# Kernel tuning notes

Hardware: AMD Instinct MI355X
Metric: run time of the kernel (lower is better)

Reference implementation:

```python
import jax, jax.numpy as jnp
import numpy as np

B, S, D = 4, 2048, 1024

def setup_inputs() -> dict:
    key = jax.random.key(0)
    k1, k2, k3, k4 = jax.random.split(key, 4)
    scale = 1.0 / np.sqrt(D)
    x = jax.random.normal(k1, (B, S, D), dtype=jnp.float32)
    Wq = jax.random.normal(k2, (D, D), dtype=jnp.float32) * scale
    Wk = jax.random.normal(k3, (D, D), dtype=jnp.float32) * scale
    Wv = jax.random.normal(k4, (D, D), dtype=jnp.float32) * scale
    return {"x": x, "Wq": Wq, "Wk": Wk, "Wv": Wv}

def reference(x, Wq, Wk, Wv):
    # Linear projections (nn.Linear with bias=False computes x @ W.T)
    q = jnp.einsum('bsd,ed->bse', x, Wq)
    k = jnp.einsum('bsd,ed->bse', x, Wk)
    v = jnp.einsum('bsd,ed->bse', x, Wv)
    # HRR binding: circular convolution of k and v == elementwise product in FFT domain
    fq = jnp.fft.fft(q, axis=-1)
    fk = jnp.fft.fft(k, axis=-1)
    fv = jnp.fft.fft(v, axis=-1)
    # Causal associative memory: cumulative sum of bound key-value pairs over sequence
    mem = jnp.cumsum(fk * fv, axis=-2)  # [B, S, D] complex
    # Unbind with query via approximate inverse (complex conjugate of fft(q))
    out = jnp.fft.ifft(mem * jnp.conj(fq), axis=-1).real
    return out.astype(x.dtype)
```

## Files before the change

kernel.cpp:

```cpp
#include <hip/hip_runtime.h>

#define BB 4
#define SS 2048
#define DD 1024
#define MM 8192
#define CH 64
#define RR 32
#define PI_F 3.14159265358979323846f

typedef __attribute__((ext_vector_type(8))) short bf16x8;
typedef __attribute__((ext_vector_type(4))) float f32x4;

__device__ __forceinline__ unsigned short f2bf(float f) {
  unsigned int u = __float_as_uint(f);
  u = (u + 0x7FFFu + ((u >> 16) & 1u)) >> 16;
  return (unsigned short)u;
}
__device__ __forceinline__ float bf2f(unsigned short h) {
  return __uint_as_float(((unsigned int)h) << 16);
}

__global__ __launch_bounds__(256) void convert_bf16(
    const float* __restrict__ src, unsigned short* __restrict__ dst) {
  const long i = ((long)blockIdx.x * 256 + threadIdx.x) * 4;
  const float4 v = *(const float4*)&src[i];
  ushort4 o;
  o.x = f2bf(v.x); o.y = f2bf(v.y); o.z = f2bf(v.z); o.w = f2bf(v.w);
  *(ushort4*)&dst[i] = o;
}

__global__ __launch_bounds__(256) void convert_w(
    const float* __restrict__ Wq, const float* __restrict__ Wk,
    const float* __restrict__ Wv, unsigned short* __restrict__ dst) {
  const int z = blockIdx.y;
  const float* src = (z == 0) ? Wq : (z == 1) ? Wk : Wv;
  const long i = ((long)blockIdx.x * 256 + threadIdx.x) * 4;
  const float4 v = *(const float4*)&src[i];
  ushort4 o;
  o.x = f2bf(v.x); o.y = f2bf(v.y); o.z = f2bf(v.z); o.w = f2bf(v.w);
  *(ushort4*)&dst[(size_t)z * DD * DD + i] = o;
}

__device__ __forceinline__ void async16(const void* g, void* l) {
  __builtin_amdgcn_global_load_lds(
      (const __attribute__((address_space(1))) void*)g,
      (__attribute__((address_space(3))) void*)l, 16, 0, 0);
}

__global__ __launch_bounds__(256) void gemm_mfma(
    const unsigned short* __restrict__ xb,
    const unsigned short* __restrict__ Wb,
    float* __restrict__ outq, unsigned short* __restrict__ KV) {
  const int z = blockIdx.z;
  const unsigned short* W = Wb + (size_t)z * DD * DD;

  __shared__ unsigned short Als[128 * 64];
  __shared__ unsigned short Bls[128 * 64];

  const int tid  = threadIdx.x;
  const int lane = tid & 63;
  const int wave = tid >> 6;
  const int wm = (wave & 1) * 64;
  const int wn = (wave >> 1) * 64;

  const long m0 = (long)blockIdx.x * 128;
  const long n0 = (long)blockIdx.y * 128;

  f32x4 acc[4][4] = {};

  for (int k0 = 0; k0 < DD; k0 += 64) {
    #pragma unroll
    for (int i = 0; i < 4; ++i) {
      const int slot = i * 256 + tid;
      const int row  = slot >> 3;
      const int kq   = slot & 7;
      const int g    = kq ^ (row & 7);
      async16(xb + (m0 + row) * DD + k0 + g * 8, &Als[slot * 8]);
      async16(W  + (n0 + row) * DD + k0 + g * 8, &Bls[slot * 8]);
    }
    __syncthreads();

    const int fr = lane & 15;
    const int kq = lane >> 4;
    #pragma unroll
    for (int h = 0; h < 2; ++h) {
      bf16x8 af[4], bfr[4];
      #pragma unroll
      for (int mt = 0; mt < 4; ++mt) {
        const int row = wm + mt * 16 + fr;
        af[mt] = *(const bf16x8*)
            &Als[row * 64 + ((((h << 2) + kq) ^ (fr & 7)) << 3)];
      }
      #pragma unroll
      for (int nt = 0; nt < 4; ++nt) {
        const int row = wn + nt * 16 + fr;
        bfr[nt] = *(const bf16x8*)
            &Bls[row * 64 + ((((h << 2) + kq) ^ (fr & 7)) << 3)];
      }
      #pragma unroll
      for (int mt = 0; mt < 4; ++mt)
        #pragma unroll
        for (int nt = 0; nt < 4; ++nt)
          acc[mt][nt] = __builtin_amdgcn_mfma_f32_16x16x32_bf16(
              af[mt], bfr[nt], acc[mt][nt], 0, 0, 0);
    }
    __syncthreads();
  }

  const int col = lane & 15;
  const int r0  = (lane >> 4) * 4;
  if (z == 0) {
    #pragma unroll
    for (int mt = 0; mt < 4; ++mt)
      #pragma unroll
      for (int nt = 0; nt < 4; ++nt)
        #pragma unroll
        for (int r = 0; r < 4; ++r) {
          const long m = m0 + wm + mt * 16 + r0 + r;
          const long n = n0 + wn + nt * 16 + col;
          outq[m * DD + n] = acc[mt][nt][r];
        }
  } else {
    unsigned short* Ck = KV + (size_t)(z - 1) * DD;
    #pragma unroll
    for (int mt = 0; mt < 4; ++mt)
      #pragma unroll
      for (int nt = 0; nt < 4; ++nt)
        #pragma unroll
        for (int r = 0; r < 4; ++r) {
          const long m = m0 + wm + mt * 16 + r0 + r;
          const long n = n0 + wn + nt * 16 + col;
          Ck[m * 2048 + n] = f2bf(acc[mt][nt][r]);
        }
  }
}

__device__ __forceinline__ int pidx(int i) { return i + (i >> 6); }
#define BUFSZ 1040
__device__ __forceinline__ int pidx16(int i) { return i + (i >> 4); }
#define MEMSZ 546

__device__ __forceinline__ int rev4(int p) {
  unsigned r = __brev((unsigned)p) >> 22;
  return (int)(((r & 0x155u) << 1) | ((r & 0x2AAu) >> 1));
}

__host__ __device__ constexpr int clog2(int s) {
  return (s == 256) ? 8 : (s == 64) ? 6 : (s == 16) ? 4 : (s == 4) ? 2 : 0;
}

template <int S>
__device__ __forceinline__ void fwd_stage(float2 x[4], int t) {
  float c1 = 1.0f, s1 = 0.0f;
  if (S > 1) {
    const int j = t & (S - 1);
    __sincosf(-2.0f * PI_F * (float)j / (float)(4 * S), &s1, &c1);
  }
  const float c2 = c1 * c1 - s1 * s1, s2 = 2.0f * c1 * s1;
  const float c3 = c1 * c2 - s1 * s2, s3 = c1 * s2 + s1 * c2;
  const float Ar = x[0].x + x[2].x, Ai = x[0].y + x[2].y;
  const float Br = x[1].x + x[3].x, Bi = x[1].y + x[3].y;
  const float Cr = x[0].x - x[2].x, Ci = x[0].y - x[2].y;
  const float dr = x[1].x - x[3].x, di = x[1].y - x[3].y;
  const float y1r = Cr + di, y1i = Ci - dr;
  const float y2r = Ar - Br, y2i = Ai - Bi;
  const float y3r = Cr - di, y3i = Ci + dr;
  x[0] = make_float2(Ar + Br, Ai + Bi);
  x[1] = make_float2(y1r * c1 - y1i * s1, y1r * s1 + y1i * c1);
  x[2] = make_float2(y2r * c2 - y2i * s2, y2r * s2 + y2i * c2);
  x[3] = make_float2(y3r * c3 - y3i * s3, y3r * s3 + y3i * c3);
}

template <int S>
__device__ __forceinline__ void inv_stage(float2 x[4], int t) {
  float c1 = 1.0f, s1 = 0.0f;
  if (S > 1) {
    const int j = t & (S - 1);
    __sincosf(2.0f * PI_F * (float)j / (float)(4 * S), &s1, &c1);
  }
  const float c2 = c1 * c1 - s1 * s1, s2 = 2.0f * c1 * s1;
  const float c3 = c1 * c2 - s1 * s2, s3 = c1 * s2 + s1 * c2;
  const float u0r = x[0].x,                   u0i = x[0].y;
  const float u1r = x[1].x * c1 - x[1].y * s1, u1i = x[1].x * s1 + x[1].y * c1;
  const float u2r = x[2].x * c2 - x[2].y * s2, u2i = x[2].x * s2 + x[2].y * c2;
  const float u3r = x[3].x * c3 - x[3].y * s3, u3i = x[3].x * s3 + x[3].y * c3;
  const float Er = u0r + u2r, Ei = u0i + u2i;
  const float Fr = u0r - u2r, Fi = u0i - u2i;
  const float Gr = u1r + u3r, Gi = u1i + u3i;
  const float Hr = u1r - u3r, Hi = u1i - u3i;
  x[0] = make_float2(Er + Gr, Ei + Gi);
  x[1] = make_float2(Fr - Hi, Fi + Hr);
  x[2] = make_float2(Er - Gr, Ei - Gi);
  x[3] = make_float2(Fr + Hi, Fi - Hr);
}

template <int SW, int SR>
__device__ __forceinline__ void xchg(float2* buf, float2 x[4], int t) {
  constexpr int LW = clog2(SW), LR = clog2(SR);
  #pragma unroll
  for (int n = 0; n < 4; ++n)
    buf[pidx(((t >> LW) << (LW + 2)) + (t & (SW - 1)) + n * SW)] = x[n];
  __syncthreads();
  #pragma unroll
  for (int n = 0; n < 4; ++n)
    x[n] = buf[pidx(((t >> LR) << (LR + 2)) + (t & (SR - 1)) + n * SR)];
  __syncthreads();
}

__device__ __forceinline__ void fwd_fft(float2* buf, float2 x[4], int t) {
  fwd_stage<256>(x, t); xchg<256, 64>(buf, x, t);
  fwd_stage<64>(x, t);  xchg<64, 16>(buf, x, t);
  fwd_stage<16>(x, t);  xchg<16, 4>(buf, x, t);
  fwd_stage<4>(x, t);   xchg<4, 1>(buf, x, t);
  fwd_stage<1>(x, t);
  #pragma unroll
  for (int n = 0; n < 4; ++n) buf[pidx(4 * t + n)] = x[n];
  __syncthreads();
}

__global__ __launch_bounds__(256) void bind_kernel(unsigned short* __restrict__ KV) {
  __shared__ float2 buf[BUFSZ];
  const int t = threadIdx.x;
  unsigned short* row = KV + (long)blockIdx.x * 2048;

  float2 x[4];
  #pragma unroll
  for (int n = 0; n < 4; ++n) {
    const int i = t + 256 * n;
    x[n] = make_float2(bf2f(row[i]), bf2f(row[1024 + i]));
  }
  fwd_fft(buf, x, t);

  float2* Prow = (float2*)row;
  #pragma unroll
  for (int m = 0; m < 2; ++m) {
    const int s = t + 256 * m;
    if (s == 0) {
      const float2 W0   = buf[pidx(0)];
      const float2 W512 = buf[pidx(2)];
      Prow[0] = make_float2(W0.x * W0.y, W512.x * W512.y);
    } else {
      const int p1 = rev4(s);
      const int p2 = rev4(1024 - s);
      const float2 F1 = buf[pidx(p1)], F2 = buf[pidx(p2)];
      const float fkr = 0.5f * (F1.x + F2.x), fki = 0.5f * (F1.y - F2.y);
      const float fvr = 0.5f * (F1.y + F2.y), fvi = 0.5f * (F2.x - F1.x);
      Prow[s] = make_float2(fkr * fvr - fki * fvi, fkr * fvi + fki * fvr);
    }
  }
}

__global__ __launch_bounds__(256) void scan_chunk_sum(
    const float2* __restrict__ P, float2* __restrict__ csum) {
  const int chunk = blockIdx.x;
  const int batch = blockIdx.y >> 1;
  const int f = (blockIdx.y & 1) * 256 + threadIdx.x;
  long base = ((long)batch * SS + (long)chunk * RR) * 512 + f;
  float sr = 0.0f, si = 0.0f;
  #pragma unroll 4
  for (int i = 0; i < RR; ++i) {
    float2 p = P[base + (long)i * 512];
    sr += p.x; si += p.y;
  }
  csum[((long)batch * CH + chunk) * 512 + f] = make_float2(sr, si);
}

__global__ __launch_bounds__(256) void scan_chunk_scan(float2* csum) {
  const int idx = blockIdx.x * 256 + threadIdx.x;
  const int batch = idx >> 9;
  const int f = idx & 511;
  float2 v[CH];
  #pragma unroll
  for (int c = 0; c < CH; ++c) v[c] = csum[((long)batch * CH + c) * 512 + f];
  float rr = 0.0f, ri = 0.0f;
  #pragma unroll
  for (int c = 0; c < CH; ++c) {
    const float2 x = v[c];
    csum[((long)batch * CH + c) * 512 + f] = make_float2(rr, ri);
    rr += x.x; ri += x.y;
  }
}

__global__ __launch_bounds__(256) void scan_apply(
    float2* __restrict__ P, const float2* __restrict__ csum) {
  const int chunk = blockIdx.x;
  const int batch = blockIdx.y >> 1;
  const int f = (blockIdx.y & 1) * 256 + threadIdx.x;
  float2 off = csum[((long)batch * CH + chunk) * 512 + f];
  float ar = off.x, ai = off.y;
  long base = ((long)batch * SS + (long)chunk * RR) * 512 + f;
  for (int i = 0; i < RR; ++i) {
    const long o = base + (long)i * 512;
    float2 p = P[o];
    ar += p.x; ai += p.y;
    P[o] = make_float2(ar, ai);
  }
}

__global__ __launch_bounds__(256) void unbind_kernel(
    float* __restrict__ qout, const float2* __restrict__ mem) {
  __shared__ float2 buf[BUFSZ];
  __shared__ float2 m0s[MEMSZ], m1s[MEMSZ];
  const int t = threadIdx.x;
  const long r0 = (long)blockIdx.x * 2;
  float* row0 = qout + r0 * DD;
  float* row1 = row0 + DD;
  const float2* mem0 = mem + r0 * 512;
  const float2* mem1 = mem0 + 512;

  float2 x[4];
  #pragma unroll
  for (int n = 0; n < 4; ++n) {
    const int i = t + 256 * n;
    x[n] = make_float2(row0[i], row1[i]);
  }
  #pragma unroll
  for (int n = 0; n < 2; ++n) {
    const int s = t + 256 * n;
    const float2 a = mem0[s], b = mem1[s];
    if (s == 0) {
      m0s[pidx16(0)]   = make_float2(a.x, 0.0f);
      m0s[pidx16(512)] = make_float2(a.y, 0.0f);
      m1s[pidx16(0)]   = make_float2(b.x, 0.0f);
      m1s[pidx16(512)] = make_float2(b.y, 0.0f);
    } else {
      m0s[pidx16(s)] = a;
      m1s[pidx16(s)] = b;
    }
  }
  fwd_fft(buf, x, t);

  float2 z[4];
  #pragma unroll
  for (int m = 0; m < 4; ++m) {
    const int p   = t + 256 * m;
    const int bin = rev4(p);
    const int p2  = rev4((1024 - bin) & 1023);
    const float2 F1 = buf[pidx(p)], F2 = buf[pidx(p2)];
    const float q0r = 0.5f * (F1.x + F2.x), q0i = 0.5f * (F1.y - F2.y);
    const float q1r = 0.5f * (F1.y + F2.y), q1i = 0.5f * (F2.x - F1.x);
    const int  ix = (bin <= 512) ? bin : 1024 - bin;
    const float sg = (bin <= 512) ? 1.0f : -1.0f;
    float2 m0 = m0s[pidx16(ix)], m1 = m1s[pidx16(ix)];
    m0.y *= sg; m1.y *= sg;
    const float z0r = m0.x * q0r + m0.y * q0i, z0i = m0.y * q0r - m0.x * q0i;
    const float z1r = m1.x * q1r + m1.y * q1i, z1i = m1.y * q1r - m1.x * q1i;
    z[m] = make_float2(z0r - z1i, z0i + z1r);
  }
  __syncthreads();
  #pragma unroll
  for (int m = 0; m < 4; ++m) buf[pidx(t + 256 * m)] = z[m];
  __syncthreads();
  #pragma unroll
  for (int n = 0; n < 4; ++n) x[n] = buf[pidx(4 * t + n)];

  inv_stage<1>(x, t);   xchg<1, 4>(buf, x, t);
  inv_stage<4>(x, t);   xchg<4, 16>(buf, x, t);
  inv_stage<16>(x, t);  xchg<16, 64>(buf, x, t);
  inv_stage<64>(x, t);  xchg<64, 256>(buf, x, t);
  inv_stage<256>(x, t);

  const float sc = 1.0f / 1024.0f;
  #pragma unroll
  for (int n = 0; n < 4; ++n) {
    const int i = t + 256 * n;
    row0[i] = x[n].x * sc;
    row1[i] = x[n].y * sc;
  }
}

extern "C" void kernel_launch(void* const* d_in, const int* in_sizes, int n_in,
                              void* d_out, int out_size, void* d_ws, size_t ws_size,
                              hipStream_t stream) {
  (void)in_sizes; (void)n_in; (void)out_size;
  const float* x  = (const float*)d_in[0];
  const float* Wq = (const float*)d_in[1];
  const float* Wk = (const float*)d_in[2];
  const float* Wv = (const float*)d_in[3];
  float* out = (float*)d_out;

  const size_t wbytes = (size_t)3 * DD * DD * 2;
  auto need = [&](size_t MHr, size_t nB) {
    return wbytes + MHr * DD * 2 + MHr * 4096 + nB * CH * 512 * 8;
  };
  const int nPass = (ws_size >= need(8192, 4)) ? 1 : 2;
  const size_t MH = MM / nPass;
  const int    nB = BB / nPass;

  char* ws = (char*)d_ws;
  unsigned short* Wb = (unsigned short*)ws;
  unsigned short* xb = (unsigned short*)(ws + wbytes);
  unsigned short* KV = (unsigned short*)(ws + wbytes + MH * DD * 2);
  float2*       csum = (float2*)((char*)KV + MH * 4096);

  convert_w<<<dim3(DD * DD / 1024, 3), 256, 0, stream>>>(Wq, Wk, Wv, Wb);

  for (int h = 0; h < nPass; ++h) {
    const float* xh   = x   + (size_t)h * MH * DD;
    float*       outh = out + (size_t)h * MH * DD;

    convert_bf16<<<MH * DD / 1024, 256, 0, stream>>>(xh, xb);
    gemm_mfma<<<dim3(MH / 128, DD / 128, 3), 256, 0, stream>>>(xb, Wb, outh, KV);
    bind_kernel<<<MH, 256, 0, stream>>>(KV);
    scan_chunk_sum<<<dim3(CH, nB * 2), 256, 0, stream>>>((const float2*)KV, csum);
    scan_chunk_scan<<<nB * 2, 256, 0, stream>>>(csum);
    scan_apply<<<dim3(CH, nB * 2), 256, 0, stream>>>((float2*)KV, csum);
    unbind_kernel<<<MH / 2, 256, 0, stream>>>(outh, (const float2*)KV);
  }
}
```

Measured before the change: 233.3 us.

## Rewrite projection GEMM as 256x256 tiles with double-buffered async LDS pipeline

The QKV projection GEMM moves from 128x128 tiles with 4 waves and a single LDS buffer to 256x256 tiles with 8 waves, 128 accumulators per wave, and a double-buffered LDS pipeline. Global-to-LDS async loads for the next K steps are interleaved with MFMA phases using explicit vmcnt/lgkmcnt waits, raw barriers, and setprio around MFMA bursts. The aim is to hide load latency and raise arithmetic intensity per LDS byte. It uses 128KB LDS per block and many registers, which limits occupancy, and correctness depends on the hand-tuned wait counts.

```diff
diff --git a/kernel.cpp b/kernel.cpp
--- a/kernel.cpp
+++ b/kernel.cpp
@@ -47,91 +47,115 @@
       (__attribute__((address_space(3))) void*)l, 16, 0, 0);
 }
 
-__global__ __launch_bounds__(256) void gemm_mfma(
+#define GW(n)  asm volatile("s_waitcnt vmcnt(" #n ")" ::: "memory")
+#define LW()   do { asm volatile("s_waitcnt lgkmcnt(0)" ::: "memory"); \
+                    __builtin_amdgcn_sched_barrier(0); } while (0)
+#define BAR()  asm volatile("s_barrier" ::: "memory")
+
+#define STA(buf, i, T) async16(xb + (size_t)(m0 + 64 * (i)) * DD + (T) * 64 + aOff, \
+                               &Als[(buf) * 16384 + (i) * 4096 + slot8])
+#define STB(buf, p, T) async16(W + (size_t)(n0 + 16 * (p)) * DD + (T) * 64 + bOff, \
+                               &Bls[(buf) * 16384 + (p) * 4096 + slot8])
+#define LDA(buf) { _Pragma("unroll") for (int mt = 0; mt < 8; ++mt) { \
+    af[mt][0] = *(const bf16x8*)&Als[(buf) * 16384 + aRd + mt * 1024 + qoff0]; \
+    af[mt][1] = *(const bf16x8*)&Als[(buf) * 16384 + aRd + mt * 1024 + qoff1]; } }
+#define LDB(buf, p) { \
+    bfv[0] = *(const bf16x8*)&Bls[(buf) * 16384 + (p) * 4096 + bRd + qoff0]; \
+    bfv[1] = *(const bf16x8*)&Bls[(buf) * 16384 + (p) * 4096 + bRd + qoff1]; }
+#define MMA(p) { __builtin_amdgcn_s_setprio(1); \
+    _Pragma("unroll") for (int mt = 0; mt < 8; ++mt) { \
+      acc[mt][p] = __builtin_amdgcn_mfma_f32_16x16x32_bf16(af[mt][0], bfv[0], acc[mt][p], 0, 0, 0); \
+      acc[mt][p] = __builtin_amdgcn_mfma_f32_16x16x32_bf16(af[mt][1], bfv[1], acc[mt][p], 0, 0, 0); } \
+    __builtin_amdgcn_s_setprio(0); }
+
+__global__ __launch_bounds__(512, 2) void gemm_mfma(
     const unsigned short* __restrict__ xb,
     const unsigned short* __restrict__ Wb,
     float* __restrict__ outq, unsigned short* __restrict__ KV) {
   const int z = blockIdx.z;
   const unsigned short* W = Wb + (size_t)z * DD * DD;
 
-  __shared__ unsigned short Als[128 * 64];
-  __shared__ unsigned short Bls[128 * 64];
+  __shared__ unsigned short Als[2 * 16384];
+  __shared__ unsigned short Bls[2 * 16384];
 
   const int tid  = threadIdx.x;
   const int lane = tid & 63;
-  const int wave = tid >> 6;
-  const int wm = (wave & 1) * 64;
-  const int wn = (wave >> 1) * 64;
-
-  const long m0 = (long)blockIdx.x * 128;
-  const long n0 = (long)blockIdx.y * 128;
-
-  f32x4 acc[4][4] = {};
-
-  for (int k0 = 0; k0 < DD; k0 += 64) {
-    #pragma unroll
-    for (int i = 0; i < 4; ++i) {
-      const int slot = i * 256 + tid;
-      const int row  = slot >> 3;
-      const int kq   = slot & 7;
-      const int g    = kq ^ (row & 7);
-      async16(xb + (m0 + row) * DD + k0 + g * 8, &Als[slot * 8]);
-      async16(W  + (n0 + row) * DD + k0 + g * 8, &Bls[slot * 8]);
-    }
-    __syncthreads();
-
-    const int fr = lane & 15;
-    const int kq = lane >> 4;
-    #pragma unroll
-    for (int h = 0; h < 2; ++h) {
-      bf16x8 af[4], bfr[4];
-      #pragma unroll
-      for (int mt = 0; mt < 4; ++mt) {
-        const int row = wm + mt * 16 + fr;
-        af[mt] = *(const bf16x8*)
-            &Als[row * 64 + ((((h << 2) + kq) ^ (fr & 7)) << 3)];
-      }
-      #pragma unroll
-      for (int nt = 0; nt < 4; ++nt) {
-        const int row = wn + nt * 16 + fr;
-        bfr[nt] = *(const bf16x8*)
-            &Bls[row * 64 + ((((h << 2) + kq) ^ (fr & 7)) << 3)];
-      }
-      #pragma unroll
-      for (int mt = 0; mt < 4; ++mt)
-        #pragma unroll
-        for (int nt = 0; nt < 4; ++nt)
-          acc[mt][nt] = __builtin_amdgcn_mfma_f32_16x16x32_bf16(
-              af[mt], bfr[nt], acc[mt][nt], 0, 0, 0);
-    }
-    __syncthreads();
-  }
+  const int w    = tid >> 6;
+  const int wm   = w >> 2;
+  const int gq   = w & 3;
+  const int fr   = lane & 15;
+  const int kq   = lane >> 4;
+
+  const int m0 = blockIdx.x * 256;
+  const int n0 = blockIdx.y * 256;
+
+  const int slot  = tid;
+  const int srow  = slot >> 3;
+  const int sq    = (slot & 7) ^ (srow & 7);
+  const int slot8 = slot * 8;
+  const size_t aOff = (size_t)srow * DD + sq * 8;
+  const size_t bOff = (size_t)(64 * (slot >> 7) + ((slot >> 3) & 15)) * DD + sq * 8;
+
+  const int qoff0 = ((0 + kq) ^ (fr & 7)) * 8;
+  const int qoff1 = ((4 + kq) ^ (fr & 7)) * 8;
+  const int aRd = wm * 8192 + fr * 64;
+  const int bRd = gq * 1024 + fr * 64;
+
+  f32x4 acc[8][4] = {};
+  bf16x8 af[8][2];
+  bf16x8 bfv[2];
+
+  STA(0, 0, 0); STA(0, 1, 0);
+  STA(0, 2, 0); STB(0, 0, 0);
+  STA(0, 3, 0); STB(0, 1, 0);
+  STB(0, 2, 0); STB(0, 3, 0);
+  STA(1, 0, 1); STA(1, 1, 1);
+  STA(1, 2, 1); STB(1, 0, 1);
+  STA(1, 3, 1); STB(1, 1, 1);
+
+  for (int T = 0; T < 14; ++T) {
+    const int buf = T & 1;
+    GW(9);  BAR(); LDA(buf); LDB(buf, 0);
+    STB(buf ^ 1, 2, T + 1); STB(buf ^ 1, 3, T + 1); LW(); MMA(0);
+    GW(10); BAR(); LDB(buf, 1);
+    STA(buf, 0, T + 2); STA(buf, 1, T + 2);         LW(); MMA(1);
+    GW(11); BAR(); LDB(buf, 2);
+    STA(buf, 2, T + 2); STB(buf, 0, T + 2);         LW(); MMA(2);
+    GW(12); BAR(); LDB(buf, 3);
+    STA(buf, 3, T + 2); STB(buf, 1, T + 2);         LW(); MMA(3);
+  }
+  GW(9);  BAR(); LDA(0); LDB(0, 0); STB(1, 2, 15); STB(1, 3, 15); LW(); MMA(0);
+  GW(10); BAR(); LDB(0, 1); LW(); MMA(1);
+  GW(9);  BAR(); LDB(0, 2); LW(); MMA(2);
+  GW(8);  BAR(); LDB(0, 3); LW(); MMA(3);
+  GW(3);  BAR(); LDA(1); LDB(1, 0); LW(); MMA(0);
+  GW(2);  BAR(); LDB(1, 1); LW(); MMA(1);
+  GW(1);  BAR(); LDB(1, 2); LW(); MMA(2);
+  GW(0);  BAR(); LDB(1, 3); LW(); MMA(3);
 
   const int col = lane & 15;
   const int r0  = (lane >> 4) * 4;
+  const int mBase = m0 + wm * 128;
+  const int nBase = n0 + gq * 64;
   if (z == 0) {
     #pragma unroll
-    for (int mt = 0; mt < 4; ++mt)
+    for (int mt = 0; mt < 8; ++mt)
       #pragma unroll
-      for (int nt = 0; nt < 4; ++nt)
+      for (int p = 0; p < 4; ++p)
         #pragma unroll
-        for (int r = 0; r < 4; ++r) {
-          const long m = m0 + wm + mt * 16 + r0 + r;
-          const long n = n0 + wn + nt * 16 + col;
-          outq[m * DD + n] = acc[mt][nt][r];
-        }
+        for (int r = 0; r < 4; ++r)
+          outq[(size_t)(mBase + mt * 16 + r0 + r) * DD + nBase + p * 16 + col] =
+              acc[mt][p][r];
   } else {
     unsigned short* Ck = KV + (size_t)(z - 1) * DD;
     #pragma unroll
-    for (int mt = 0; mt < 4; ++mt)
+    for (int mt = 0; mt < 8; ++mt)
       #pragma unroll
-      for (int nt = 0; nt < 4; ++nt)
+      for (int p = 0; p < 4; ++p)
         #pragma unroll
-        for (int r = 0; r < 4; ++r) {
-          const long m = m0 + wm + mt * 16 + r0 + r;
-          const long n = n0 + wn + nt * 16 + col;
-          Ck[m * 2048 + n] = f2bf(acc[mt][nt][r]);
-        }
+        for (int r = 0; r < 4; ++r)
+          Ck[(size_t)(mBase + mt * 16 + r0 + r) * 2048 + nBase + p * 16 + col] =
+              f2bf(acc[mt][p][r]);
   }
 }
 
@@ -196,10 +220,10 @@
 
 template <int SW, int SR>
 __device__ __forceinline__ void xchg(float2* buf, float2 x[4], int t) {
-  constexpr int LW = clog2(SW), LR = clog2(SR);
+  constexpr int LW2 = clog2(SW), LR = clog2(SR);
   #pragma unroll
   for (int n = 0; n < 4; ++n)
-    buf[pidx(((t >> LW) << (LW + 2)) + (t & (SW - 1)) + n * SW)] = x[n];
+    buf[pidx(((t >> LW2) << (LW2 + 2)) + (t & (SW - 1)) + n * SW)] = x[n];
   __syncthreads();
   #pragma unroll
   for (int n = 0; n < 4; ++n)
@@ -400,7 +424,7 @@
     float*       outh = out + (size_t)h * MH * DD;
 
     convert_bf16<<<MH * DD / 1024, 256, 0, stream>>>(xh, xb);
-    gemm_mfma<<<dim3(MH / 128, DD / 128, 3), 256, 0, stream>>>(xb, Wb, outh, KV);
+    gemm_mfma<<<dim3(MH / 256, DD / 256, 3), dim3(512), 0, stream>>>(xb, Wb, outh, KV);
     bind_kernel<<<MH, 256, 0, stream>>>(KV);
     scan_chunk_sum<<<dim3(CH, nB * 2), 256, 0, stream>>>((const float2*)KV, csum);
     scan_chunk_scan<<<nB * 2, 256, 0, stream>>>(csum);
```

Measured after the change: 238.6 us. +2.3%, slower.
